# Kernel tuning notes

Hardware: AMD Instinct MI355X
Metric: run time of the kernel (lower is better)

The kernel has to match this reference:

```python
import jax, jax.numpy as jnp
import numpy as np
import math

B, S, D = 8, 2048, 1024

def setup_inputs() -> dict:
    key = jax.random.key(0)
    ks = jax.random.split(key, 9)
    scale = 1.0 / math.sqrt(D)
    Q = jax.random.normal(ks[0], (B, S, D), dtype=jnp.float32)
    K = jax.random.normal(ks[1], (B, S, D), dtype=jnp.float32)
    V = jax.random.normal(ks[2], (B, S, D), dtype=jnp.float32)
    Wq = jax.random.normal(ks[3], (D, D), dtype=jnp.float32) * scale
    Wk = jax.random.normal(ks[4], (D, D), dtype=jnp.float32) * scale
    Wv = jax.random.normal(ks[5], (D, D), dtype=jnp.float32) * scale
    bq = jnp.zeros((D,), dtype=jnp.float32)
    bk = jnp.zeros((D,), dtype=jnp.float32)
    bv = jnp.zeros((D,), dtype=jnp.float32)
    # causal mask, broadcast over batch: [1, S, S]
    mask = jnp.tril(jnp.ones((S, S), dtype=jnp.int32))[None, :, :]
    return {"Q": Q, "K": K, "V": V, "Wq": Wq, "Wk": Wk, "Wv": Wv,
            "bq": bq, "bk": bk, "bv": bv, "mask": mask}

def reference(Q, K, V, Wq, Wk, Wv, bq, bk, bv, mask):
    d_model = Q.shape[-1]
    q = jnp.einsum('bsd,de->bse', Q, Wq) + bq
    k = jnp.einsum('bsd,de->bse', K, Wk) + bk
    v = jnp.einsum('bsd,de->bse', V, Wv) + bv
    scores = jnp.einsum('bqd,bkd->bqk', q, k) / math.sqrt(d_model)  # [B,S,S]
    scores = jnp.where(mask == 0, jnp.float32(-1e9), scores)
    weights = jax.nn.softmax(scores, axis=-1)
    out = jnp.einsum('bqk,bkd->bqd', weights, v)
    return out
```

## Files before the change

### kernel.cpp

```cpp
#include <hip/hip_runtime.h>
#include <hip/hip_bf16.h>

#define Bb 8
#define Ss 2048
#define Dd 1024

typedef short bf16x8 __attribute__((ext_vector_type(8)));
typedef float f32x4  __attribute__((ext_vector_type(4)));

__device__ __forceinline__ short f2bf(float f) {
  union { __hip_bfloat16 h; short s; } u;
  u.h = __float2bfloat16(f);
  return u.s;
}
__device__ __forceinline__ float bf2f(short s) {
  union { unsigned int u; float f; } v;
  v.u = ((unsigned int)(unsigned short)s) << 16;
  return v.f;
}

__device__ __forceinline__ int swz(int row, int slot) {
  return row * 64 + (((slot ^ row) & 7) << 3);
}
__device__ __forceinline__ int swzp(int r, int lk) {
  int R = r >> 1;
  int slot = ((r & 1) << 2) | lk;
  return R * 64 + (((slot ^ R) & 7) << 3);
}

__device__ __forceinline__ void gld16(const short* g, short* l) {
  __builtin_amdgcn_global_load_lds((const __attribute__((address_space(1))) void*)g,
                                   (__attribute__((address_space(3))) void*)l, 16, 0, 0);
}

__device__ __forceinline__ void stage_glds(const short* __restrict__ src, int ld,
                                           short* lds, int tid) {
  int w = tid >> 6;
#pragma unroll
  for (int it = 0; it < 4; ++it) {
    int u = it * 256 + tid;
    int r = u >> 3;
    int ssrc = (u ^ r) & 7;
    const short* g = src + (size_t)r * ld + ssrc * 8;
    short* lbase = lds + (size_t)(it * 256 + w * 64) * 8;
    gld16(g, lbase);
  }
}

__device__ __forceinline__ void stage_packed(const short* __restrict__ src, int ld,
                                             short* lds, int tid) {
  int w = tid >> 6;
#pragma unroll
  for (int it = 0; it < 2; ++it) {
    int u = it * 512 + tid;
    int R = u >> 3, slotL = u & 7;
    int pre = slotL ^ (R & 7);
    int r = (R << 1) | (pre >> 2);
    int kc = pre & 3;
    const short* g = src + (size_t)r * ld + kc * 8;
    short* lbase = lds + (size_t)(it * 512 + w * 64) * 8;
    gld16(g, lbase);
  }
}

__device__ __forceinline__ void mfma_tile(const short* ldsA, const short* ldsB,
                                          f32x4 acc[4][4], int wm, int wn, int lr, int lk) {
#pragma unroll
  for (int c = 0; c < 2; ++c) {
    bf16x8 afr[4], bfr[4];
#pragma unroll
    for (int m = 0; m < 4; ++m)
      afr[m] = *(const bf16x8*)&ldsA[swz(wm * 64 + m * 16 + lr, c * 4 + lk)];
#pragma unroll
    for (int n = 0; n < 4; ++n)
      bfr[n] = *(const bf16x8*)&ldsB[swz(wn * 64 + n * 16 + lr, c * 4 + lk)];
#pragma unroll
    for (int m = 0; m < 4; ++m)
#pragma unroll
      for (int n = 0; n < 4; ++n)
        acc[m][n] = __builtin_amdgcn_mfma_f32_16x16x32_bf16(afr[m], bfr[n], acc[m][n], 0, 0, 0);
  }
}

__global__ void wcast_kernel(const float* __restrict__ Wq, const float* __restrict__ Wk,
                             const float* __restrict__ Wv,
                             short* __restrict__ WtQ, short* __restrict__ WtK,
                             short* __restrict__ WtV) {
  int z = blockIdx.z;
  const float* W = (z == 0) ? Wq : (z == 1) ? Wk : Wv;
  short* Wt      = (z == 0) ? WtQ : (z == 1) ? WtK : WtV;
  __shared__ float tile[32][33];
  int r0 = blockIdx.y * 32, c0 = blockIdx.x * 32;
  int tx = threadIdx.x, ty = threadIdx.y;
#pragma unroll
  for (int ii = 0; ii < 4; ++ii) {
    int r = ty * 4 + ii;
    tile[r][tx] = W[(size_t)(r0 + r) * Dd + c0 + tx];
  }
  __syncthreads();
#pragma unroll
  for (int ii = 0; ii < 4; ++ii) {
    int c = ty * 4 + ii;
    Wt[(size_t)(c0 + c) * Dd + r0 + tx] = f2bf(tile[tx][c]);
  }
}

__global__ void cast_kernel(const float* __restrict__ src, short* __restrict__ dst) {
  size_t i = (size_t)blockIdx.x * blockDim.x + threadIdx.x;
  size_t stride = (size_t)gridDim.x * blockDim.x;
  const size_t N8 = (size_t)Bb * Ss * Dd / 8;
  for (; i < N8; i += stride) {
    float4 a = ((const float4*)src)[2 * i];
    float4 b = ((const float4*)src)[2 * i + 1];
    bf16x8 h;
    h[0] = f2bf(a.x); h[1] = f2bf(a.y); h[2] = f2bf(a.z); h[3] = f2bf(a.w);
    h[4] = f2bf(b.x); h[5] = f2bf(b.y); h[6] = f2bf(b.z); h[7] = f2bf(b.w);
    *(bf16x8*)(dst + i * 8) = h;
  }
}

#define NT 32
__launch_bounds__(512, 2)
__global__ void proj8_kernel(const short* __restrict__ A, const short* __restrict__ W,
                             const float* __restrict__ bias, short* __restrict__ out,
                             int tmode) {
  __shared__ short lds[3][2][128 * 64];
  int g = blockIdx.x;
  int xcd = g & 7, j = g >> 3;
  int nblk = j & 3, mp = j >> 2;
  int mblk = mp * 8 + xcd;
  int m0 = mblk * 256, n0 = nblk * 256;

  int tid = threadIdx.x;
  int lane = tid & 63, w = tid >> 6;
  int wm = w >> 2, wn = w & 3;
  int lr = lane & 15, lk = lane >> 4;

  const short* Ab = A + (size_t)m0 * Dd;
  const short* Wb = W + (size_t)n0 * Dd;

  f32x4 acc[8][4] = {};

  stage_packed(Ab + 0, Dd, lds[0][0], tid);
  stage_packed(Wb + 0, Dd, lds[0][1], tid);
  stage_packed(Ab + 32, Dd, lds[1][0], tid);
  stage_packed(Wb + 32, Dd, lds[1][1], tid);
  asm volatile("s_waitcnt vmcnt(4)" ::: "memory");
  __builtin_amdgcn_s_barrier();
  __builtin_amdgcn_sched_barrier(0);

  for (int t = 0; t < NT; ++t) {
    const short* la = lds[t % 3][0];
    const short* lb = lds[t % 3][1];
    bool pf = (t + 2) < NT;
    short* pa = lds[(t + 2) % 3][0];
    short* pb = lds[(t + 2) % 3][1];
    int kpre = (t + 2) * 32;

    bf16x8 bfr[4], afr[4];
#pragma unroll
    for (int n = 0; n < 4; ++n)
      bfr[n] = *(const bf16x8*)&lb[swzp(wn * 64 + n * 16 + lr, lk)];
#pragma unroll
    for (int m = 0; m < 4; ++m)
      afr[m] = *(const bf16x8*)&la[swzp(wm * 128 + m * 16 + lr, lk)];
    if (pf) stage_packed(Ab + kpre, Dd, pa, tid);
    __builtin_amdgcn_s_barrier();
    __builtin_amdgcn_sched_barrier(0);
    __builtin_amdgcn_s_setprio(1);
#pragma unroll
    for (int m = 0; m < 4; ++m)
#pragma unroll
      for (int n = 0; n < 4; ++n)
        acc[m][n] = __builtin_amdgcn_mfma_f32_16x16x32_bf16(afr[m], bfr[n], acc[m][n], 0, 0, 0);
    __builtin_amdgcn_s_setprio(0);
    __builtin_amdgcn_s_barrier();
    __builtin_amdgcn_sched_barrier(0);
#pragma unroll
    for (int m = 0; m < 4; ++m)
      afr[m] = *(const bf16x8*)&la[swzp(wm * 128 + 64 + m * 16 + lr, lk)];
    if (pf) stage_packed(Wb + kpre, Dd, pb, tid);
    __builtin_amdgcn_s_barrier();
    __builtin_amdgcn_sched_barrier(0);
    __builtin_amdgcn_s_setprio(1);
#pragma unroll
    for (int m = 0; m < 4; ++m)
#pragma unroll
      for (int n = 0; n < 4; ++n)
        acc[4 + m][n] = __builtin_amdgcn_mfma_f32_16x16x32_bf16(afr[m], bfr[n], acc[4 + m][n], 0, 0, 0);
    __builtin_amdgcn_s_setprio(0);
    if (pf)                asm volatile("s_waitcnt vmcnt(4)" ::: "memory");
    else if (t + 1 < NT)   asm volatile("s_waitcnt vmcnt(0)" ::: "memory");
    __builtin_amdgcn_s_barrier();
    __builtin_amdgcn_sched_barrier(0);
  }

#pragma unroll
  for (int m = 0; m < 8; ++m) {
    int mrow = wm * 128 + (m >> 2) * 64 + (m & 3) * 16 + lk * 4;
#pragma unroll
    for (int n = 0; n < 4; ++n) {
      int col = n0 + wn * 64 + n * 16 + lr;
      float bv_ = bias[col];
      if (tmode == 0) {
        int rbase = m0 + mrow;
#pragma unroll
        for (int rr = 0; rr < 4; ++rr)
          out[(size_t)(rbase + rr) * Dd + col] = f2bf(acc[m][n][rr] + bv_);
      } else {
        int grow = m0 + mrow;
        int bidx = grow / Ss;
        int s0 = grow & (Ss - 1);
        short4 h;
        h.x = f2bf(acc[m][n][0] + bv_);
        h.y = f2bf(acc[m][n][1] + bv_);
        h.z = f2bf(acc[m][n][2] + bv_);
        h.w = f2bf(acc[m][n][3] + bv_);
        *(short4*)&out[(size_t)bidx * Dd * Ss + (size_t)col * Ss + s0] = h;
      }
    }
  }
}

__launch_bounds__(256, 4)
__global__ void score_kernel(const short* __restrict__ qb, const short* __restrict__ kb,
                             short* __restrict__ SP) {
  int d = blockIdx.x;
  int b = d & 7;
  int sidx = d >> 3;
  int i = (int)((sqrtf(8.f * sidx + 1.f) - 1.f) * 0.5f);
  while ((i + 1) * (i + 2) / 2 <= sidx) ++i;
  while (i * (i + 1) / 2 > sidx) --i;
  int j = sidx - i * (i + 1) / 2;

  __shared__ short ldsA[128 * 64];
  __shared__ short ldsB[128 * 64];
  int tid = threadIdx.x;
  int lane = tid & 63, w = tid >> 6;
  int wm = w >> 1, wn = w & 1;
  int lr = lane & 15, lk = lane >> 4;

  const short* Abase = qb + (size_t)b * Ss * Dd + (size_t)i * 128 * Dd;
  const short* Bbase = kb + (size_t)b * Ss * Dd + (size_t)j * 128 * Dd;

  f32x4 acc[4][4] = {};
  for (int k0 = 0; k0 < Dd; k0 += 64) {
    __syncthreads();
    stage_glds(Abase + k0, Dd, ldsA, tid);
    stage_glds(Bbase + k0, Dd, ldsB, tid);
    __syncthreads();
    mfma_tile(ldsA, ldsB, acc, wm, wn, lr, lk);
  }

  short* srow = SP + (size_t)b * Ss * Ss;
#pragma unroll
  for (int m = 0; m < 4; ++m)
#pragma unroll
    for (int n = 0; n < 4; ++n) {
      int colg = j * 128 + wn * 64 + n * 16 + lr;
      int rbase = i * 128 + wm * 64 + m * 16 + lk * 4;
#pragma unroll
      for (int rr = 0; rr < 4; ++rr) {
        int rowg = rbase + rr;
        float sv = acc[m][n][rr] * 0.03125f;
        if (colg > rowg) sv = -1e9f;
        srow[(size_t)rowg * Ss + colg] = f2bf(sv);
      }
    }
}

__global__ void softmax_kernel(short* __restrict__ SP) {
  int row = blockIdx.x;
  int b = row >> 11;
  int q = row & (Ss - 1);
  int L = ((q >> 7) + 1) << 7;
  short* srow = SP + (size_t)b * Ss * Ss + (size_t)q * Ss;
  int tid = threadIdx.x;
  int lane = tid & 63, w = tid >> 6;

  float vals[8];
  int cnt = 0;
  float mx = -3.0e38f;
  for (int c = tid; c < L; c += 256) {
    float f = bf2f(srow[c]);
    vals[cnt++] = f;
    mx = fmaxf(mx, f);
  }
  __shared__ float red[8];
#pragma unroll
  for (int off = 32; off; off >>= 1) mx = fmaxf(mx, __shfl_xor(mx, off));
  if (lane == 0) red[w] = mx;
  __syncthreads();
  mx = fmaxf(fmaxf(red[0], red[1]), fmaxf(red[2], red[3]));

  float sum = 0.f;
  for (int k2 = 0; k2 < cnt; ++k2) {
    float e = __expf(vals[k2] - mx);
    vals[k2] = e;
    sum += e;
  }
#pragma unroll
  for (int off = 32; off; off >>= 1) sum += __shfl_xor(sum, off);
  if (lane == 0) red[4 + w] = sum;
  __syncthreads();
  sum = red[4] + red[5] + red[6] + red[7];
  float inv = 1.0f / sum;

  cnt = 0;
  for (int c = tid; c < L; c += 256) srow[c] = f2bf(vals[cnt++] * inv);
}

__launch_bounds__(256, 4)
__global__ void pv_kernel(const short* __restrict__ SP, const short* __restrict__ vT,
                          float* __restrict__ out) {
  int d = blockIdx.x;
  int b = d & 7;
  int s = d >> 3;
  int i = s >> 3;
  int dblk = s & 7;

  __shared__ short ldsA[128 * 64];
  __shared__ short ldsB[128 * 64];
  int tid = threadIdx.x;
  int lane = tid & 63, w = tid >> 6;
  int wm = w >> 1, wn = w & 1;
  int lr = lane & 15, lk = lane >> 4;

  const short* Abase = SP + (size_t)b * Ss * Ss + (size_t)i * 128 * Ss;
  const short* Bbase = vT + (size_t)b * Dd * Ss + (size_t)dblk * 128 * Ss;
  int KL = (i + 1) * 128;

  f32x4 acc[4][4] = {};
  for (int k0 = 0; k0 < KL; k0 += 64) {
    __syncthreads();
    stage_glds(Abase + k0, Ss, ldsA, tid);
    stage_glds(Bbase + k0, Ss, ldsB, tid);
    __syncthreads();
    mfma_tile(ldsA, ldsB, acc, wm, wn, lr, lk);
  }

#pragma unroll
  for (int m = 0; m < 4; ++m)
#pragma unroll
    for (int n = 0; n < 4; ++n) {
      int colg = dblk * 128 + wn * 64 + n * 16 + lr;
      int rbase = i * 128 + wm * 64 + m * 16 + lk * 4;
#pragma unroll
      for (int rr = 0; rr < 4; ++rr)
        out[(size_t)b * Ss * Dd + (size_t)(rbase + rr) * Dd + colg] = acc[m][n][rr];
    }
}

extern "C" void kernel_launch(void* const* d_in, const int* in_sizes, int n_in,
                              void* d_out, int out_size, void* d_ws, size_t ws_size,
                              hipStream_t stream) {
  const float* Q  = (const float*)d_in[0];
  const float* K  = (const float*)d_in[1];
  const float* V  = (const float*)d_in[2];
  const float* Wq = (const float*)d_in[3];
  const float* Wk = (const float*)d_in[4];
  const float* Wv = (const float*)d_in[5];
  const float* bq = (const float*)d_in[6];
  const float* bk = (const float*)d_in[7];
  const float* bv = (const float*)d_in[8];
  float* out = (float*)d_out;

  char* ws = (char*)d_ws;
  size_t off = 0;
  short* WtQ = (short*)(ws + off); off += (size_t)Dd * Dd * 2;
  short* WtK = (short*)(ws + off); off += (size_t)Dd * Dd * 2;
  short* WtV = (short*)(ws + off); off += (size_t)Dd * Dd * 2;
  short* qb  = (short*)(ws + off); off += (size_t)Bb * Ss * Dd * 2;
  short* kb  = (short*)(ws + off); off += (size_t)Bb * Ss * Dd * 2;
  short* vT  = (short*)(ws + off); off += (size_t)Bb * Ss * Dd * 2;
  short* SP  = (short*)(ws + off); off += (size_t)Bb * Ss * Ss * 2;
  short* Xbf = SP;
  (void)ws_size; (void)in_sizes; (void)n_in; (void)out_size;

  wcast_kernel<<<dim3(32, 32, 3), dim3(32, 8), 0, stream>>>(Wq, Wk, Wv, WtQ, WtK, WtV);

  cast_kernel<<<1024, 256, 0, stream>>>(Q, Xbf);
  proj8_kernel<<<256, 512, 0, stream>>>(Xbf, WtQ, bq, qb, 0);
  cast_kernel<<<1024, 256, 0, stream>>>(K, Xbf);
  proj8_kernel<<<256, 512, 0, stream>>>(Xbf, WtK, bk, kb, 0);
  cast_kernel<<<1024, 256, 0, stream>>>(V, Xbf);
  proj8_kernel<<<256, 512, 0, stream>>>(Xbf, WtV, bv, vT, 1);

  score_kernel<<<dim3(1088), 256, 0, stream>>>(qb, kb, SP);
  softmax_kernel<<<dim3(Bb * Ss), 256, 0, stream>>>(SP);
  pv_kernel<<<dim3(1024), 256, 0, stream>>>(SP, vT, out);
}
```

Before: 328.1 us.

## Fuse fp32-to-bf16 cast into batched QKV projection and vectorize softmax

Removes the three standalone cast kernels: the projection kernel now stages fp32 activations straight into LDS and converts them to bf16 in registers before the MFMAs. The three projections are merged into one launch using blockIdx.y. The per-iteration pipeline is reordered so both prefetches are issued up front with fewer barriers. Softmax switches to one 16-byte vector load and store per thread. The trade-off is doubled LDS for the A tile, which may lower occupancy, plus extra conversion ALU work inside the GEMM loop.

```diff
diff --git a/kernel.cpp b/kernel.cpp
--- a/kernel.cpp
+++ b/kernel.cpp
@@ -27,8 +27,13 @@
   int slot = ((r & 1) << 2) | lk;
   return R * 64 + (((slot ^ R) & 7) << 3);
 }
-
-__device__ __forceinline__ void gld16(const short* g, short* l) {
+__device__ __forceinline__ int swzpf(int r, int kc4) {
+  int R = r >> 1;
+  int slot = ((r & 1) << 3) | kc4;
+  return R * 64 + ((slot ^ (R & 15)) << 2);
+}
+
+__device__ __forceinline__ void gld16(const void* g, void* l) {
   __builtin_amdgcn_global_load_lds((const __attribute__((address_space(1))) void*)g,
                                    (__attribute__((address_space(3))) void*)l, 16, 0, 0);
 }
@@ -41,9 +46,7 @@
     int u = it * 256 + tid;
     int r = u >> 3;
     int ssrc = (u ^ r) & 7;
-    const short* g = src + (size_t)r * ld + ssrc * 8;
-    short* lbase = lds + (size_t)(it * 256 + w * 64) * 8;
-    gld16(g, lbase);
+    gld16(src + (size_t)r * ld + ssrc * 8, lds + (size_t)(it * 256 + w * 64) * 8);
   }
 }
 
@@ -57,9 +60,21 @@
     int pre = slotL ^ (R & 7);
     int r = (R << 1) | (pre >> 2);
     int kc = pre & 3;
-    const short* g = src + (size_t)r * ld + kc * 8;
-    short* lbase = lds + (size_t)(it * 512 + w * 64) * 8;
-    gld16(g, lbase);
+    gld16(src + (size_t)r * ld + kc * 8, lds + (size_t)(it * 512 + w * 64) * 8);
+  }
+}
+
+__device__ __forceinline__ void stage_packed_f32(const float* __restrict__ src, int ld,
+                                                 float* lds, int tid) {
+  int w = tid >> 6;
+#pragma unroll
+  for (int it = 0; it < 4; ++it) {
+    int u = it * 512 + tid;
+    int R = u >> 4, slotL = u & 15;
+    int pre = slotL ^ (R & 15);
+    int r = (R << 1) | (pre >> 3);
+    int kc4 = pre & 7;
+    gld16(src + (size_t)r * ld + kc4 * 4, lds + (size_t)(it * 512 + w * 64) * 4);
   }
 }
 
@@ -105,26 +120,23 @@
   }
 }
 
-__global__ void cast_kernel(const float* __restrict__ src, short* __restrict__ dst) {
-  size_t i = (size_t)blockIdx.x * blockDim.x + threadIdx.x;
-  size_t stride = (size_t)gridDim.x * blockDim.x;
-  const size_t N8 = (size_t)Bb * Ss * Dd / 8;
-  for (; i < N8; i += stride) {
-    float4 a = ((const float4*)src)[2 * i];
-    float4 b = ((const float4*)src)[2 * i + 1];
-    bf16x8 h;
-    h[0] = f2bf(a.x); h[1] = f2bf(a.y); h[2] = f2bf(a.z); h[3] = f2bf(a.w);
-    h[4] = f2bf(b.x); h[5] = f2bf(b.y); h[6] = f2bf(b.z); h[7] = f2bf(b.w);
-    *(bf16x8*)(dst + i * 8) = h;
-  }
-}
-
 #define NT 32
 __launch_bounds__(512, 2)
-__global__ void proj8_kernel(const short* __restrict__ A, const short* __restrict__ W,
-                             const float* __restrict__ bias, short* __restrict__ out,
-                             int tmode) {
-  __shared__ short lds[3][2][128 * 64];
+__global__ void proj8_kernel(const float* __restrict__ Q, const float* __restrict__ Kin,
+                             const float* __restrict__ V,
+                             const short* __restrict__ WtQ, const short* __restrict__ WtK,
+                             const short* __restrict__ WtV,
+                             const float* __restrict__ bq, const float* __restrict__ bk,
+                             const float* __restrict__ bv,
+                             short* __restrict__ qb, short* __restrict__ kb,
+                             short* __restrict__ vT) {
+  __shared__ float ldsA[3][128 * 64];
+  __shared__ short ldsB[3][128 * 64];
+  int z = blockIdx.y;
+  const float* A    = (z == 0) ? Q : (z == 1) ? Kin : V;
+  const short* W    = (z == 0) ? WtQ : (z == 1) ? WtK : WtV;
+  const float* bias = (z == 0) ? bq : (z == 1) ? bk : bv;
+
   int g = blockIdx.x;
   int xcd = g & 7, j = g >> 3;
   int nblk = j & 3, mp = j >> 2;
@@ -136,63 +148,67 @@
   int wm = w >> 2, wn = w & 3;
   int lr = lane & 15, lk = lane >> 4;
 
-  const short* Ab = A + (size_t)m0 * Dd;
+  const float* Ab = A + (size_t)m0 * Dd;
   const short* Wb = W + (size_t)n0 * Dd;
 
   f32x4 acc[8][4] = {};
 
-  stage_packed(Ab + 0, Dd, lds[0][0], tid);
-  stage_packed(Wb + 0, Dd, lds[0][1], tid);
-  stage_packed(Ab + 32, Dd, lds[1][0], tid);
-  stage_packed(Wb + 32, Dd, lds[1][1], tid);
-  asm volatile("s_waitcnt vmcnt(4)" ::: "memory");
+  stage_packed_f32(Ab + 0, Dd, ldsA[0], tid);
+  stage_packed(Wb + 0, Dd, ldsB[0], tid);
+  stage_packed_f32(Ab + 32, Dd, ldsA[1], tid);
+  stage_packed(Wb + 32, Dd, ldsB[1], tid);
+  asm volatile("s_waitcnt vmcnt(6)" ::: "memory");
   __builtin_amdgcn_s_barrier();
-  __builtin_amdgcn_sched_barrier(0);
+  asm volatile("" ::: "memory");
 
   for (int t = 0; t < NT; ++t) {
-    const short* la = lds[t % 3][0];
-    const short* lb = lds[t % 3][1];
+    const float* la = ldsA[t % 3];
+    const short* lb = ldsB[t % 3];
     bool pf = (t + 2) < NT;
-    short* pa = lds[(t + 2) % 3][0];
-    short* pb = lds[(t + 2) % 3][1];
-    int kpre = (t + 2) * 32;
-
-    bf16x8 bfr[4], afr[4];
+    if (pf) {
+      stage_packed_f32(Ab + (t + 2) * 32, Dd, ldsA[(t + 2) % 3], tid);
+      stage_packed(Wb + (t + 2) * 32, Dd, ldsB[(t + 2) % 3], tid);
+    }
+    bf16x8 bfr[4], afr0[4], afr1[4];
 #pragma unroll
     for (int n = 0; n < 4; ++n)
       bfr[n] = *(const bf16x8*)&lb[swzp(wn * 64 + n * 16 + lr, lk)];
 #pragma unroll
+    for (int m = 0; m < 4; ++m) {
+      int r0r = wm * 128 + m * 16 + lr;
+      f32x4 a0 = *(const f32x4*)&la[swzpf(r0r, lk * 2)];
+      f32x4 a1 = *(const f32x4*)&la[swzpf(r0r, lk * 2 + 1)];
+      bf16x8 h;
+      h[0] = f2bf(a0[0]); h[1] = f2bf(a0[1]); h[2] = f2bf(a0[2]); h[3] = f2bf(a0[3]);
+      h[4] = f2bf(a1[0]); h[5] = f2bf(a1[1]); h[6] = f2bf(a1[2]); h[7] = f2bf(a1[3]);
+      afr0[m] = h;
+    }
+#pragma unroll
+    for (int m = 0; m < 4; ++m) {
+      int r1r = wm * 128 + 64 + m * 16 + lr;
+      f32x4 a0 = *(const f32x4*)&la[swzpf(r1r, lk * 2)];
+      f32x4 a1 = *(const f32x4*)&la[swzpf(r1r, lk * 2 + 1)];
+      bf16x8 h;
+      h[0] = f2bf(a0[0]); h[1] = f2bf(a0[1]); h[2] = f2bf(a0[2]); h[3] = f2bf(a0[3]);
+      h[4] = f2bf(a1[0]); h[5] = f2bf(a1[1]); h[6] = f2bf(a1[2]); h[7] = f2bf(a1[3]);
+      afr1[m] = h;
+    }
+    __builtin_amdgcn_s_setprio(1);
+#pragma unroll
     for (int m = 0; m < 4; ++m)
-      afr[m] = *(const bf16x8*)&la[swzp(wm * 128 + m * 16 + lr, lk)];
-    if (pf) stage_packed(Ab + kpre, Dd, pa, tid);
-    __builtin_amdgcn_s_barrier();
-    __builtin_amdgcn_sched_barrier(0);
-    __builtin_amdgcn_s_setprio(1);
+#pragma unroll
+      for (int n = 0; n < 4; ++n)
+        acc[m][n] = __builtin_amdgcn_mfma_f32_16x16x32_bf16(afr0[m], bfr[n], acc[m][n], 0, 0, 0);
 #pragma unroll
     for (int m = 0; m < 4; ++m)
 #pragma unroll
       for (int n = 0; n < 4; ++n)
-        acc[m][n] = __builtin_amdgcn_mfma_f32_16x16x32_bf16(afr[m], bfr[n], acc[m][n], 0, 0, 0);
+        acc[4 + m][n] = __builtin_amdgcn_mfma_f32_16x16x32_bf16(afr1[m], bfr[n], acc[4 + m][n], 0, 0, 0);
     __builtin_amdgcn_s_setprio(0);
-    __builtin_amdgcn_s_barrier();
-    __builtin_amdgcn_sched_barrier(0);
-#pragma unroll
-    for (int m = 0; m < 4; ++m)
-      afr[m] = *(const bf16x8*)&la[swzp(wm * 128 + 64 + m * 16 + lr, lk)];
-    if (pf) stage_packed(Wb + kpre, Dd, pb, tid);
-    __builtin_amdgcn_s_barrier();
-    __builtin_amdgcn_sched_barrier(0);
-    __builtin_amdgcn_s_setprio(1);
-#pragma unroll
-    for (int m = 0; m < 4; ++m)
-#pragma unroll
-      for (int n = 0; n < 4; ++n)
-        acc[4 + m][n] = __builtin_amdgcn_mfma_f32_16x16x32_bf16(afr[m], bfr[n], acc[4 + m][n], 0, 0, 0);
-    __builtin_amdgcn_s_setprio(0);
-    if (pf)                asm volatile("s_waitcnt vmcnt(4)" ::: "memory");
+    if (pf)                asm volatile("s_waitcnt vmcnt(6)" ::: "memory");
     else if (t + 1 < NT)   asm volatile("s_waitcnt vmcnt(0)" ::: "memory");
     __builtin_amdgcn_s_barrier();
-    __builtin_amdgcn_sched_barrier(0);
+    asm volatile("" ::: "memory");
   }
 
 #pragma unroll
@@ -202,7 +218,8 @@
     for (int n = 0; n < 4; ++n) {
       int col = n0 + wn * 64 + n * 16 + lr;
       float bv_ = bias[col];
-      if (tmode == 0) {
+      if (z < 2) {
+        short* out = (z == 0) ? qb : kb;
         int rbase = m0 + mrow;
 #pragma unroll
         for (int rr = 0; rr < 4; ++rr)
@@ -216,7 +233,7 @@
         h.y = f2bf(acc[m][n][1] + bv_);
         h.z = f2bf(acc[m][n][2] + bv_);
         h.w = f2bf(acc[m][n][3] + bv_);
-        *(short4*)&out[(size_t)bidx * Dd * Ss + (size_t)col * Ss + s0] = h;
+        *(short4*)&vT[(size_t)bidx * Dd * Ss + (size_t)col * Ss + s0] = h;
       }
     }
   }
@@ -277,14 +294,18 @@
   short* srow = SP + (size_t)b * Ss * Ss + (size_t)q * Ss;
   int tid = threadIdx.x;
   int lane = tid & 63, w = tid >> 6;
-
-  float vals[8];
-  int cnt = 0;
+  int c8 = tid * 8;
+  bool act = c8 < L;
+
+  float v[8];
   float mx = -3.0e38f;
-  for (int c = tid; c < L; c += 256) {
-    float f = bf2f(srow[c]);
-    vals[cnt++] = f;
-    mx = fmaxf(mx, f);
+  if (act) {
+    bf16x8 hv = *(const bf16x8*)&srow[c8];
+#pragma unroll
+    for (int j2 = 0; j2 < 8; ++j2) {
+      v[j2] = bf2f(hv[j2]);
+      mx = fmaxf(mx, v[j2]);
+    }
   }
   __shared__ float red[8];
 #pragma unroll
@@ -294,10 +315,12 @@
   mx = fmaxf(fmaxf(red[0], red[1]), fmaxf(red[2], red[3]));
 
   float sum = 0.f;
-  for (int k2 = 0; k2 < cnt; ++k2) {
-    float e = __expf(vals[k2] - mx);
-    vals[k2] = e;
-    sum += e;
+  if (act) {
+#pragma unroll
+    for (int j2 = 0; j2 < 8; ++j2) {
+      v[j2] = __expf(v[j2] - mx);
+      sum += v[j2];
+    }
   }
 #pragma unroll
   for (int off = 32; off; off >>= 1) sum += __shfl_xor(sum, off);
@@ -306,8 +329,12 @@
   sum = red[4] + red[5] + red[6] + red[7];
   float inv = 1.0f / sum;
 
-  cnt = 0;
-  for (int c = tid; c < L; c += 256) srow[c] = f2bf(vals[cnt++] * inv);
+  if (act) {
+    bf16x8 ho;
+#pragma unroll
+    for (int j2 = 0; j2 < 8; ++j2) ho[j2] = f2bf(v[j2] * inv);
+    *(bf16x8*)&srow[c8] = ho;
+  }
 }
 
 __launch_bounds__(256, 4)
@@ -374,18 +401,11 @@
   short* kb  = (short*)(ws + off); off += (size_t)Bb * Ss * Dd * 2;
   short* vT  = (short*)(ws + off); off += (size_t)Bb * Ss * Dd * 2;
   short* SP  = (short*)(ws + off); off += (size_t)Bb * Ss * Ss * 2;
-  short* Xbf = SP;
   (void)ws_size; (void)in_sizes; (void)n_in; (void)out_size;
 
   wcast_kernel<<<dim3(32, 32, 3), dim3(32, 8), 0, stream>>>(Wq, Wk, Wv, WtQ, WtK, WtV);
-
-  cast_kernel<<<1024, 256, 0, stream>>>(Q, Xbf);
-  proj8_kernel<<<256, 512, 0, stream>>>(Xbf, WtQ, bq, qb, 0);
-  cast_kernel<<<1024, 256, 0, stream>>>(K, Xbf);
-  proj8_kernel<<<256, 512, 0, stream>>>(Xbf, WtK, bk, kb, 0);
-  cast_kernel<<<1024, 256, 0, stream>>>(V, Xbf);
-  proj8_kernel<<<256, 512, 0, stream>>>(Xbf, WtV, bv, vT, 1);
-
+  proj8_kernel<<<dim3(256, 3), 512, 0, stream>>>(Q, K, V, WtQ, WtK, WtV, bq, bk, bv,
+                                                 qb, kb, vT);
   score_kernel<<<dim3(1088), 256, 0, stream>>>(qb, kb, SP);
   softmax_kernel<<<dim3(Bb * Ss), 256, 0, stream>>>(SP);
   pv_kernel<<<dim3(1024), 256, 0, stream>>>(SP, vT, out);
```

Result: slower. 342.7 us (+4.5%).

## Issue GEMM prefetch up front with fewer barriers; vectorize softmax rows

Applied to the files above, without the earlier changes.

In the triple-buffered projection GEMM loop, both A and W tile prefetches for step t+2 are now issued at the start of each iteration. Four of the five per-iteration barriers and their sched_barriers are removed, leaving one barrier at the end of each iteration. The softmax kernel now has each thread load and store 8 contiguous bf16 values as a single 16-byte vector, replacing the strided scalar loop. The aim is to cut synchronisation overhead in the GEMM and memory instruction count in softmax. The cost is less explicit interleaving of MFMA work with LDS reads and loads.

```diff
diff --git a/kernel.cpp b/kernel.cpp
--- a/kernel.cpp
+++ b/kernel.cpp
@@ -28,7 +28,7 @@
   return R * 64 + (((slot ^ R) & 7) << 3);
 }
 
-__device__ __forceinline__ void gld16(const short* g, short* l) {
+__device__ __forceinline__ void gld16(const void* g, void* l) {
   __builtin_amdgcn_global_load_lds((const __attribute__((address_space(1))) void*)g,
                                    (__attribute__((address_space(3))) void*)l, 16, 0, 0);
 }
@@ -41,9 +41,7 @@
     int u = it * 256 + tid;
     int r = u >> 3;
     int ssrc = (u ^ r) & 7;
-    const short* g = src + (size_t)r * ld + ssrc * 8;
-    short* lbase = lds + (size_t)(it * 256 + w * 64) * 8;
-    gld16(g, lbase);
+    gld16(src + (size_t)r * ld + ssrc * 8, lds + (size_t)(it * 256 + w * 64) * 8);
   }
 }
 
@@ -57,9 +55,7 @@
     int pre = slotL ^ (R & 7);
     int r = (R << 1) | (pre >> 2);
     int kc = pre & 3;
-    const short* g = src + (size_t)r * ld + kc * 8;
-    short* lbase = lds + (size_t)(it * 512 + w * 64) * 8;
-    gld16(g, lbase);
+    gld16(src + (size_t)r * ld + kc * 8, lds + (size_t)(it * 512 + w * 64) * 8);
   }
 }
 
@@ -141,22 +137,21 @@
 
   f32x4 acc[8][4] = {};
 
-  stage_packed(Ab + 0, Dd, lds[0][0], tid);
-  stage_packed(Wb + 0, Dd, lds[0][1], tid);
+  stage_packed(Ab + 0,  Dd, lds[0][0], tid);
+  stage_packed(Wb + 0,  Dd, lds[0][1], tid);
   stage_packed(Ab + 32, Dd, lds[1][0], tid);
   stage_packed(Wb + 32, Dd, lds[1][1], tid);
   asm volatile("s_waitcnt vmcnt(4)" ::: "memory");
   __builtin_amdgcn_s_barrier();
-  __builtin_amdgcn_sched_barrier(0);
 
   for (int t = 0; t < NT; ++t) {
     const short* la = lds[t % 3][0];
     const short* lb = lds[t % 3][1];
     bool pf = (t + 2) < NT;
-    short* pa = lds[(t + 2) % 3][0];
-    short* pb = lds[(t + 2) % 3][1];
-    int kpre = (t + 2) * 32;
-
+    if (pf) {
+      stage_packed(Ab + (t + 2) * 32, Dd, lds[(t + 2) % 3][0], tid);
+      stage_packed(Wb + (t + 2) * 32, Dd, lds[(t + 2) % 3][1], tid);
+    }
     bf16x8 bfr[4], afr[4];
 #pragma unroll
     for (int n = 0; n < 4; ++n)
@@ -164,9 +159,6 @@
 #pragma unroll
     for (int m = 0; m < 4; ++m)
       afr[m] = *(const bf16x8*)&la[swzp(wm * 128 + m * 16 + lr, lk)];
-    if (pf) stage_packed(Ab + kpre, Dd, pa, tid);
-    __builtin_amdgcn_s_barrier();
-    __builtin_amdgcn_sched_barrier(0);
     __builtin_amdgcn_s_setprio(1);
 #pragma unroll
     for (int m = 0; m < 4; ++m)
@@ -174,14 +166,9 @@
       for (int n = 0; n < 4; ++n)
         acc[m][n] = __builtin_amdgcn_mfma_f32_16x16x32_bf16(afr[m], bfr[n], acc[m][n], 0, 0, 0);
     __builtin_amdgcn_s_setprio(0);
-    __builtin_amdgcn_s_barrier();
-    __builtin_amdgcn_sched_barrier(0);
 #pragma unroll
     for (int m = 0; m < 4; ++m)
       afr[m] = *(const bf16x8*)&la[swzp(wm * 128 + 64 + m * 16 + lr, lk)];
-    if (pf) stage_packed(Wb + kpre, Dd, pb, tid);
-    __builtin_amdgcn_s_barrier();
-    __builtin_amdgcn_sched_barrier(0);
     __builtin_amdgcn_s_setprio(1);
 #pragma unroll
     for (int m = 0; m < 4; ++m)
@@ -191,8 +178,7 @@
     __builtin_amdgcn_s_setprio(0);
     if (pf)                asm volatile("s_waitcnt vmcnt(4)" ::: "memory");
     else if (t + 1 < NT)   asm volatile("s_waitcnt vmcnt(0)" ::: "memory");
-    __builtin_amdgcn_s_barrier();
-    __builtin_amdgcn_sched_barrier(0);
+    if (t + 1 < NT) __builtin_amdgcn_s_barrier();
   }
 
 #pragma unroll
@@ -277,14 +263,18 @@
   short* srow = SP + (size_t)b * Ss * Ss + (size_t)q * Ss;
   int tid = threadIdx.x;
   int lane = tid & 63, w = tid >> 6;
-
-  float vals[8];
-  int cnt = 0;
+  int c8 = tid * 8;
+  bool act = c8 < L;
+
+  float v[8];
   float mx = -3.0e38f;
-  for (int c = tid; c < L; c += 256) {
-    float f = bf2f(srow[c]);
-    vals[cnt++] = f;
-    mx = fmaxf(mx, f);
+  if (act) {
+    bf16x8 hv = *(const bf16x8*)&srow[c8];
+#pragma unroll
+    for (int j2 = 0; j2 < 8; ++j2) {
+      v[j2] = bf2f(hv[j2]);
+      mx = fmaxf(mx, v[j2]);
+    }
   }
   __shared__ float red[8];
 #pragma unroll
@@ -294,10 +284,12 @@
   mx = fmaxf(fmaxf(red[0], red[1]), fmaxf(red[2], red[3]));
 
   float sum = 0.f;
-  for (int k2 = 0; k2 < cnt; ++k2) {
-    float e = __expf(vals[k2] - mx);
-    vals[k2] = e;
-    sum += e;
+  if (act) {
+#pragma unroll
+    for (int j2 = 0; j2 < 8; ++j2) {
+      v[j2] = __expf(v[j2] - mx);
+      sum += v[j2];
+    }
   }
 #pragma unroll
   for (int off = 32; off; off >>= 1) sum += __shfl_xor(sum, off);
@@ -306,8 +298,12 @@
   sum = red[4] + red[5] + red[6] + red[7];
   float inv = 1.0f / sum;
 
-  cnt = 0;
-  for (int c = tid; c < L; c += 256) srow[c] = f2bf(vals[cnt++] * inv);
+  if (act) {
+    bf16x8 ho;
+#pragma unroll
+    for (int j2 = 0; j2 < 8; ++j2) ho[j2] = f2bf(v[j2] * inv);
+    *(bf16x8*)&srow[c8] = ho;
+  }
 }
 
 __launch_bounds__(256, 4)
```

New measurement: 301.1 us. 1.09x faster.
